# Kernel optimization log

Measured on AMD Instinct MI355X. Metric: run time of the kernel, lower is better.

## Reference

```python
import jax, jax.numpy as jnp
import numpy as np

N = 16384          # batch of signals
DIM_T = 256        # time steps per signal
DT = 0.01          # integration dt (intg_lev=1 -> dt_intg = dt)
NUF = 256          # num_units_feat
HID_XI = 128       # hidlayers_xi
HID_AUX = 64       # hidlayers_aux1_dec
LEN_INTG = DIM_T   # (dim_t-1)*intg_lev + 1 with intg_lev=1


def _linear_init(key, fan_in, fan_out):
    # torch nn.Linear default: U(-1/sqrt(fan_in), 1/sqrt(fan_in))
    s = 1.0 / np.sqrt(fan_in)
    kw, kb = jax.random.split(key)
    W = jax.random.uniform(kw, (fan_in, fan_out), minval=-s, maxval=s, dtype=jnp.float32)
    b = jax.random.uniform(kb, (fan_out,), minval=-s, maxval=s, dtype=jnp.float32)
    return W, b


def setup_inputs() -> dict:
    key = jax.random.key(0)
    ks = jax.random.split(key, 12)
    data = jax.random.normal(ks[0], (N, DIM_T), dtype=jnp.float32)
    omega = jax.random.normal(ks[1], (N, 1), dtype=jnp.float32)
    eps = jax.random.normal(ks[2], (N, 1), dtype=jnp.float32)
    # feature extractor (mlp branch): [dim_t+1 -> 256 -> 256], relu after both (actfun_output=True)
    W_feat1, b_feat1 = _linear_init(ks[3], DIM_T + 1, NUF)
    W_feat2, b_feat2 = _linear_init(ks[4], NUF, NUF)
    # xi mean head: MLP [256 -> 128 -> 1] then Softplus
    W_xim1, b_xim1 = _linear_init(ks[5], NUF, HID_XI)
    W_xim2, b_xim2 = _linear_init(ks[6], HID_XI, 1)
    # xi lnvar head: MLP [256 -> 128 -> 1]
    W_xil1, b_xil1 = _linear_init(ks[7], NUF, HID_XI)
    W_xil2, b_xil2 = _linear_init(ks[8], HID_XI, 1)
    # decoder aux1 MLP: [dim_z_aux1+1=2 -> 64 -> 1]
    W_aux1, b_aux1 = _linear_init(ks[9], 2, HID_AUX)
    W_aux2, b_aux2 = _linear_init(ks[10], HID_AUX, 1)
    return dict(data=data, omega=omega, eps=eps,
                W_feat1=W_feat1, b_feat1=b_feat1, W_feat2=W_feat2, b_feat2=b_feat2,
                W_xim1=W_xim1, b_xim1=b_xim1, W_xim2=W_xim2, b_xim2=b_xim2,
                W_xil1=W_xil1, b_xil1=b_xil1, W_xil2=W_xil2, b_xil2=b_xil2,
                W_aux1=W_aux1, b_aux1=b_aux1, W_aux2=W_aux2, b_aux2=b_aux2)


def reference(data, omega, eps,
              W_feat1, b_feat1, W_feat2, b_feat2,
              W_xim1, b_xim1, W_xim2, b_xim2,
              W_xil1, b_xil1, W_xil2, b_xil2,
              W_aux1, b_aux1, W_aux2, b_aux2):
    relu = jax.nn.relu
    # ---- encode_xi ----
    x_ = jnp.concatenate([data, omega], axis=1)                 # [n, dim_t+1]
    feat = relu(relu(x_ @ W_feat1 + b_feat1) @ W_feat2 + b_feat2)  # [n, 256]
    xi_mean = jax.nn.softplus(relu(feat @ W_xim1 + b_xim1) @ W_xim2 + b_xim2)  # [n, 1]
    xi_lnvar = relu(feat @ W_xil1 + b_xil1) @ W_xil2 + b_xil2                  # [n, 1]
    # ---- draw (reparameterization + clamp to feasible range [0, 1]) ----
    xi = xi_mean + jnp.exp(0.5 * xi_lnvar) * eps
    xi = jnp.clip(xi, 0.0, 1.0)
    # ---- decode: Euler odeint over LEN_INTG steps of state yy=[y, dy/dt] ----
    init_y = data[:, :1]                                        # [n, 1]
    initcond = jnp.concatenate([init_y, jnp.zeros_like(init_y)], axis=1)  # [n, 2]

    def step(yy, _):
        # physics: d[y, v]/dt = [v, 0]; aux MLP adds acceleration from (z_aux1=omega, y)
        aux_in = jnp.concatenate([omega, yy[:, :1]], axis=1)    # [n, 2]
        acc = relu(aux_in @ W_aux1 + b_aux1) @ W_aux2 + b_aux2  # [n, 1]
        dyy = jnp.concatenate([yy[:, 1:2], acc], axis=1)        # [n, 2]
        return yy + DT * dyy, yy

    _, yy_seq = jax.lax.scan(step, initcond, None, length=LEN_INTG)  # [len_intg, n, 2]
    y_seq = yy_seq[:, :, 0].T                                   # [n, dim_t] (intg_lev=1)
    t_intg = DT * jnp.arange(LEN_INTG, dtype=jnp.float32)       # [dim_t]
    x_PAB = jnp.exp(-jnp.abs(xi) * t_intg[None, :]) * y_seq     # [n, dim_t]
    return xi_mean, xi_lnvar, x_PAB
```

## Files before the change

kernel.cpp:

```cpp
#include <hip/hip_runtime.h>
#include <math.h>

#define NROWS 16384
#define DT_C 0.01f

typedef short s16x8 __attribute__((ext_vector_type(8)));
typedef float f32x4 __attribute__((ext_vector_type(4)));
typedef float f32x2 __attribute__((ext_vector_type(2)));

__device__ __forceinline__ unsigned short f2bf(float f) {
    unsigned u = __float_as_uint(f);
    u += 0x7fffu + ((u >> 16) & 1u);
    return (unsigned short)(u >> 16);
}
__device__ __forceinline__ unsigned pack2bf(float a, float b) {
    return (unsigned)f2bf(a) | ((unsigned)f2bf(b) << 16);
}
template <int CTRL>
__device__ __forceinline__ float dppadd(float v) {
    int x = __builtin_amdgcn_update_dpp(0, __float_as_int(v), CTRL, 0xF, 0xF, true);
    return v + __int_as_float(x);
}
__device__ __forceinline__ float sum4(float p) {
    p = dppadd<0xB1>(p);
    p = dppadd<0x4E>(p);
    return p;
}
__device__ __forceinline__ float sum8(float p) {
    p = dppadd<0xB1>(p);
    p = dppadd<0x4E>(p);
    p = dppadd<0x141>(p);
    return p;
}

__global__ __launch_bounds__(256) void prep_k(
    const float* __restrict__ Wf1, const float* __restrict__ Wf2,
    const float* __restrict__ Wm1, const float* __restrict__ Wl1,
    const float* __restrict__ bm1, const float* __restrict__ bl1,
    unsigned short* __restrict__ wpack, float* __restrict__ biasH)
{
    const int id = blockIdx.x * 256 + threadIdx.x;
    const int n  = id & 255;
    const int k8 = (id >> 8) & 31;
    const int s  = id >> 13;

    unsigned short tmp[8];
    #pragma unroll
    for (int j = 0; j < 8; ++j) {
        const int k = k8 * 8 + j;
        float v;
        if (s == 0)      v = Wf1[k * 256 + n];
        else if (s == 1) v = Wf2[k * 256 + n];
        else             v = (n < 128) ? Wm1[k * 128 + n] : Wl1[k * 128 + n - 128];
        tmp[j] = f2bf(v);
    }
    *(uint4*)&wpack[((s * 32 + k8) * 256 + n) * 8] = *(const uint4*)tmp;

    if (id < 256) biasH[id] = (id < 128) ? bm1[id] : bl1[id - 128];
}

__global__ __launch_bounds__(256, 2) void mega_k(
    const float* __restrict__ data, const float* __restrict__ omega,
    const float* __restrict__ eps_g,
    const unsigned short* __restrict__ wpack, const float* __restrict__ biasH,
    const float* __restrict__ bf1, const float* __restrict__ bf2,
    const float* __restrict__ w256g,
    const float* __restrict__ Wm2, const float* __restrict__ bm2,
    const float* __restrict__ Wl2, const float* __restrict__ bl2,
    float* __restrict__ out_mean, float* __restrict__ out_lnvar,
    float* __restrict__ xi_ws)
{
    __shared__ __align__(16) unsigned char smem[32896];
    unsigned short* As1 = (unsigned short*)smem;
    unsigned short* Hs  = (unsigned short*)(smem + 16384);
    float* headsF = (float*)smem;
    float* omg = (float*)(smem + 32768);

    const int tid  = threadIdx.x;
    const int wid  = tid >> 6;
    const int lane = tid & 63;
    const int ln   = lane & 15;
    const int quad = lane >> 4;
    const int r0   = blockIdx.x * 32;

    {
        #pragma unroll
        for (int g2 = 0; g2 < 8; ++g2) {
            const int unit = g2 * 256 + tid;
            const int m    = unit >> 6;
            const int c16  = unit & 63;
            const int kblk = c16 >> 1;
            const int h    = c16 & 1;
            const float4 v = *(const float4*)&data[(size_t)(r0 + m) * 256 + c16 * 4];
            unsigned* d = (unsigned*)&As1[((kblk * 32) + (m ^ (kblk & 7))) * 8 + h * 4];
            d[0] = pack2bf(v.x, v.y);
            d[1] = pack2bf(v.z, v.w);
        }
        if (tid < 32) omg[tid] = omega[r0 + tid];
    }

    f32x4 acc[2][4];

    auto seed = [&](const float* bias) {
        #pragma unroll
        for (int nt = 0; nt < 4; ++nt) {
            const float b = bias[wid * 64 + nt * 16 + ln];
            acc[0][nt] = f32x4{b, b, b, b};
            acc[1][nt] = acc[0][nt];
        }
    };

    auto run_stage = [&](const unsigned short* Ap, const unsigned short* wp) {
        #pragma unroll
        for (int c = 0; c < 4; ++c) {
            #pragma unroll
            for (int kk = 0; kk < 2; ++kk) {
                const int kb   = kk * 4 + quad;
                const int kblk = c * 8 + kb;
                const int f    = kblk & 7;
                s16x8 b0 = *(const s16x8*)&wp[((size_t)(kblk * 256) + wid * 64 + 0 * 16 + ln) * 8];
                s16x8 b1 = *(const s16x8*)&wp[((size_t)(kblk * 256) + wid * 64 + 1 * 16 + ln) * 8];
                s16x8 b2 = *(const s16x8*)&wp[((size_t)(kblk * 256) + wid * 64 + 2 * 16 + ln) * 8];
                s16x8 b3 = *(const s16x8*)&wp[((size_t)(kblk * 256) + wid * 64 + 3 * 16 + ln) * 8];
                s16x8 a0 = *(const s16x8*)&Ap[(kblk * 32 + (ln ^ f)) * 8];
                s16x8 a1 = *(const s16x8*)&Ap[(kblk * 32 + ((ln ^ f) + 16)) * 8];
                acc[0][0] = __builtin_amdgcn_mfma_f32_16x16x32_bf16(a0, b0, acc[0][0], 0, 0, 0);
                acc[1][0] = __builtin_amdgcn_mfma_f32_16x16x32_bf16(a1, b0, acc[1][0], 0, 0, 0);
                acc[0][1] = __builtin_amdgcn_mfma_f32_16x16x32_bf16(a0, b1, acc[0][1], 0, 0, 0);
                acc[1][1] = __builtin_amdgcn_mfma_f32_16x16x32_bf16(a1, b1, acc[1][1], 0, 0, 0);
                acc[0][2] = __builtin_amdgcn_mfma_f32_16x16x32_bf16(a0, b2, acc[0][2], 0, 0, 0);
                acc[1][2] = __builtin_amdgcn_mfma_f32_16x16x32_bf16(a1, b2, acc[1][2], 0, 0, 0);
                acc[0][3] = __builtin_amdgcn_mfma_f32_16x16x32_bf16(a0, b3, acc[0][3], 0, 0, 0);
                acc[1][3] = __builtin_amdgcn_mfma_f32_16x16x32_bf16(a1, b3, acc[1][3], 0, 0, 0);
            }
        }
    };

    auto write_packed = [&](unsigned short* dst, bool addOm) {
        #pragma unroll
        for (int nt = 0; nt < 4; ++nt) {
            const int col = wid * 64 + nt * 16 + ln;
            const int kg  = col >> 3, f = kg & 7, jj = col & 7;
            const float wo = addOm ? w256g[col] : 0.f;
            #pragma unroll
            for (int mt = 0; mt < 2; ++mt) {
                #pragma unroll
                for (int r = 0; r < 4; ++r) {
                    const int row = mt * 16 + quad * 4 + r;
                    float v = acc[mt][nt][r];
                    if (addOm) v = fmaf(omg[row], wo, v);
                    v = fmaxf(v, 0.f);
                    dst[(kg * 32 + (row ^ f)) * 8 + jj] = f2bf(v);
                }
            }
        }
    };

    __syncthreads();
    seed(bf1);
    run_stage(As1, wpack);
    write_packed(Hs, true);
    __syncthreads();
    seed(bf2);
    run_stage(Hs, wpack + 65536);
    write_packed(As1, false);
    __syncthreads();
    seed(biasH);
    run_stage(As1, wpack + 131072);
    __syncthreads();
    #pragma unroll
    for (int nt = 0; nt < 4; ++nt) {
        const int col = wid * 64 + nt * 16 + ln;
        #pragma unroll
        for (int mt = 0; mt < 2; ++mt) {
            #pragma unroll
            for (int r = 0; r < 4; ++r) {
                const int row = mt * 16 + quad * 4 + r;
                headsF[row * 256 + ((col + row * 8) & 255)] = fmaxf(acc[mt][nt][r], 0.f);
            }
        }
    }
    __syncthreads();

    {
        const int m = tid >> 3, l = tid & 7;
        float pm = 0.f, pl = 0.f;
        #pragma unroll
        for (int q = 0; q < 4; ++q) {
            const int c0 = l * 16 + q * 4;
            const float4 hm = *(const float4*)&headsF[m * 256 + ((c0 + m * 8) & 255)];
            const float4 wm = *(const float4*)&Wm2[c0];
            const float4 hl = *(const float4*)&headsF[m * 256 + ((128 + c0 + m * 8) & 255)];
            const float4 wl = *(const float4*)&Wl2[c0];
            pm = fmaf(hm.w, wm.w, fmaf(hm.z, wm.z, fmaf(hm.y, wm.y, fmaf(hm.x, wm.x, pm))));
            pl = fmaf(hl.w, wl.w, fmaf(hl.z, wl.z, fmaf(hl.y, wl.y, fmaf(hl.x, wl.x, pl))));
        }
        pm = sum8(pm);
        pl = sum8(pl);
        if (l == 0) {
            const float xm   = pm + bm2[0];
            const float mean = fmaxf(xm, 0.f) + log1pf(expf(-fabsf(xm)));
            const float lnv  = pl + bl2[0];
            out_mean[r0 + m]  = mean;
            out_lnvar[r0 + m] = lnv;
            float xi = mean + expf(0.5f * lnv) * eps_g[r0 + m];
            xi_ws[r0 + m] = fminf(fmaxf(xi, 0.f), 1.f);
        }
    }
}

__global__ __launch_bounds__(256) void ode2_k(
    const float* __restrict__ data, const float* __restrict__ omega_g,
    const float* __restrict__ xi_ws,
    const float* __restrict__ Wa1, const float* __restrict__ ba1,
    const float* __restrict__ Wa2, const float* __restrict__ ba2,
    float* __restrict__ xout)
{
    const int tid = threadIdx.x;
    const int r   = tid >> 2;
    const int l   = tid & 3;
    const int row = blockIdx.x * 64 + r;

    const float om = omega_g[row];
    const float xi = xi_ws[row];
    const float s  = expf(-xi * DT_C);
    const float pseed = ba2[0] * 0.25f;

    f32x2 w1v[8], Av[8], w2v[8];
    #pragma unroll
    for (int i = 0; i < 8; ++i) {
        const int u = l * 16 + i * 2;
        const f32x2 w0 = *(const f32x2*)&Wa1[u];
        const f32x2 bb = *(const f32x2*)&ba1[u];
        w1v[i] = *(const f32x2*)&Wa1[64 + u];
        w2v[i] = *(const f32x2*)&Wa2[u];
        Av[i]  = f32x2{fmaf(om, w0.x, bb.x), fmaf(om, w0.y, bb.y)};
    }

    auto partial = [&](float y) -> float {
        const f32x2 y2 = f32x2{y, y};
        f32x2 a0 = f32x2{pseed, 0.f};
        f32x2 a1 = f32x2{0.f, 0.f};
        f32x2 a2 = f32x2{0.f, 0.f};
        f32x2 a3 = f32x2{0.f, 0.f};
        #pragma unroll
        for (int i = 0; i < 8; ++i) {
            f32x2 h = __builtin_elementwise_fma(y2, w1v[i], Av[i]);
            h = __builtin_elementwise_max(h, f32x2{0.f, 0.f});
            if ((i & 3) == 0) a0 = __builtin_elementwise_fma(h, w2v[i], a0);
            if ((i & 3) == 1) a1 = __builtin_elementwise_fma(h, w2v[i], a1);
            if ((i & 3) == 2) a2 = __builtin_elementwise_fma(h, w2v[i], a2);
            if ((i & 3) == 3) a3 = __builtin_elementwise_fma(h, w2v[i], a3);
        }
        a0 = a0 + a1;
        a2 = a2 + a3;
        a0 = a0 + a2;
        return a0.x + a0.y;
    };

    const float y0 = data[(size_t)row * 256];
    float ym = y0;
    float yc = y0;
    const float DT2 = DT_C * DT_C;
    float pr = sum4(partial(ym));
    float d = 1.f;

    float* orow = xout + (size_t)row * 256 + l * 4;
    for (int b = 0; b < 16; ++b) {
        float cur[4] = {0.f, 0.f, 0.f, 0.f};
        #pragma unroll
        for (int j = 0; j < 16; ++j) {
            const float m_ = d * ym;
            if ((j >> 2) == l) cur[j & 3] = m_;
            d *= s;
            float pn = sum4(partial(yc));
            const float ynext = fmaf(DT2, pr, fmaf(2.f, yc, -ym));
            ym = yc; yc = ynext; pr = pn;
        }
        *(float4*)&orow[b * 16] = *(const float4*)cur;
    }
}

extern "C" void kernel_launch(void* const* d_in, const int* in_sizes, int n_in,
                              void* d_out, int out_size, void* d_ws, size_t ws_size,
                              hipStream_t stream)
{
    const float* data    = (const float*)d_in[0];
    const float* omega   = (const float*)d_in[1];
    const float* eps     = (const float*)d_in[2];
    const float* W_feat1 = (const float*)d_in[3];
    const float* b_feat1 = (const float*)d_in[4];
    const float* W_feat2 = (const float*)d_in[5];
    const float* b_feat2 = (const float*)d_in[6];
    const float* W_xim1  = (const float*)d_in[7];
    const float* b_xim1  = (const float*)d_in[8];
    const float* W_xim2  = (const float*)d_in[9];
    const float* b_xim2  = (const float*)d_in[10];
    const float* W_xil1  = (const float*)d_in[11];
    const float* b_xil1  = (const float*)d_in[12];
    const float* W_xil2  = (const float*)d_in[13];
    const float* b_xil2  = (const float*)d_in[14];
    const float* W_aux1  = (const float*)d_in[15];
    const float* b_aux1  = (const float*)d_in[16];
    const float* W_aux2  = (const float*)d_in[17];
    const float* b_aux2  = (const float*)d_in[18];

    float* out_mean  = (float*)d_out;
    float* out_lnvar = out_mean + NROWS;
    float* out_x     = out_lnvar + NROWS;

    unsigned short* wpack = (unsigned short*)d_ws;
    float* biasH = (float*)((char*)d_ws + 3 * 32 * 256 * 8 * 2);
    float* xi_ws = biasH + 256;

    prep_k<<<96, 256, 0, stream>>>(W_feat1, W_feat2, W_xim1, W_xil1,
                                   b_xim1, b_xil1, wpack, biasH);
    mega_k<<<512, 256, 0, stream>>>(data, omega, eps, wpack, biasH,
                                    b_feat1, b_feat2, W_feat1 + 256 * 256,
                                    W_xim2, b_xim2, W_xil2, b_xil2,
                                    out_mean, out_lnvar, xi_ws);
    ode2_k<<<256, 256, 0, stream>>>(data, omega, xi_ws,
                                    W_aux1, b_aux1, W_aux2, b_aux2, out_x);
}
```

Before: 141.1 us.

## Fuse ODE and encoder kernels, overlapping ODE integration with MLP via atomic counter

Merges the encoder MLP kernel and the ODE integration kernel into one launch. The first 256 blocks integrate the ODE independently of xi and buffer the trajectory in registers. They then spin on a global counter until all 512 encoder blocks have published xi, and apply the exponential decay at write time. This is meant to overlap the serial ODE recurrence with the GEMM work and remove a kernel launch boundary. The cost is higher register pressure from holding 64 values per thread, and a risk of deadlock if the waiting blocks occupy every slot before the encoder blocks get scheduled.

Result: slower. 151.8 us (+7.6%).

```diff
diff --git a/kernel.cpp b/kernel.cpp
--- a/kernel.cpp
+++ b/kernel.cpp
@@ -3,6 +3,8 @@
 
 #define NROWS 16384
 #define DT_C 0.01f
+#define ODE_BLOCKS 256
+#define MEGA_BLOCKS 512
 
 typedef short s16x8 __attribute__((ext_vector_type(8)));
 typedef float f32x4 __attribute__((ext_vector_type(4)));
@@ -37,7 +39,8 @@
     const float* __restrict__ Wf1, const float* __restrict__ Wf2,
     const float* __restrict__ Wm1, const float* __restrict__ Wl1,
     const float* __restrict__ bm1, const float* __restrict__ bl1,
-    unsigned short* __restrict__ wpack, float* __restrict__ biasH)
+    unsigned short* __restrict__ wpack, float* __restrict__ biasH,
+    unsigned* __restrict__ cnt)
 {
     const int id = blockIdx.x * 256 + threadIdx.x;
     const int n  = id & 255;
@@ -57,9 +60,10 @@
     *(uint4*)&wpack[((s * 32 + k8) * 256 + n) * 8] = *(const uint4*)tmp;
 
     if (id < 256) biasH[id] = (id < 128) ? bm1[id] : bl1[id - 128];
-}
-
-__global__ __launch_bounds__(256, 2) void mega_k(
+    if (id == 0)  *cnt = 0u;
+}
+
+__global__ __launch_bounds__(256, 2) void fat_k(
     const float* __restrict__ data, const float* __restrict__ omega,
     const float* __restrict__ eps_g,
     const unsigned short* __restrict__ wpack, const float* __restrict__ biasH,
@@ -67,21 +71,110 @@
     const float* __restrict__ w256g,
     const float* __restrict__ Wm2, const float* __restrict__ bm2,
     const float* __restrict__ Wl2, const float* __restrict__ bl2,
+    const float* __restrict__ Wa1, const float* __restrict__ ba1,
+    const float* __restrict__ Wa2, const float* __restrict__ ba2,
     float* __restrict__ out_mean, float* __restrict__ out_lnvar,
-    float* __restrict__ xi_ws)
+    float* __restrict__ xi_ws, unsigned* __restrict__ cnt,
+    float* __restrict__ xout)
 {
     __shared__ __align__(16) unsigned char smem[32896];
+
+    const int tid = threadIdx.x;
+
+    if (blockIdx.x < ODE_BLOCKS) {
+        const int r   = tid >> 2;
+        const int l   = tid & 3;
+        const int row = blockIdx.x * 64 + r;
+
+        const float om = omega[row];
+        const float pseed = ba2[0] * 0.25f;
+
+        f32x2 w1v[8], Av[8], w2v[8];
+        #pragma unroll
+        for (int i = 0; i < 8; ++i) {
+            const int u = l * 16 + i * 2;
+            const f32x2 w0 = *(const f32x2*)&Wa1[u];
+            const f32x2 bb = *(const f32x2*)&ba1[u];
+            w1v[i] = *(const f32x2*)&Wa1[64 + u];
+            w2v[i] = *(const f32x2*)&Wa2[u];
+            Av[i]  = f32x2{fmaf(om, w0.x, bb.x), fmaf(om, w0.y, bb.y)};
+        }
+
+        auto partial = [&](float y) -> float {
+            const f32x2 y2 = f32x2{y, y};
+            f32x2 a0 = f32x2{pseed, 0.f};
+            f32x2 a1 = f32x2{0.f, 0.f};
+            f32x2 a2 = f32x2{0.f, 0.f};
+            f32x2 a3 = f32x2{0.f, 0.f};
+            #pragma unroll
+            for (int i = 0; i < 8; ++i) {
+                f32x2 h = __builtin_elementwise_fma(y2, w1v[i], Av[i]);
+                h = __builtin_elementwise_max(h, f32x2{0.f, 0.f});
+                if ((i & 3) == 0) a0 = __builtin_elementwise_fma(h, w2v[i], a0);
+                if ((i & 3) == 1) a1 = __builtin_elementwise_fma(h, w2v[i], a1);
+                if ((i & 3) == 2) a2 = __builtin_elementwise_fma(h, w2v[i], a2);
+                if ((i & 3) == 3) a3 = __builtin_elementwise_fma(h, w2v[i], a3);
+            }
+            a0 = a0 + a1;
+            a2 = a2 + a3;
+            a0 = a0 + a2;
+            return a0.x + a0.y;
+        };
+
+        float cur[16][4];
+        const float y0 = data[(size_t)row * 256];
+        float ym = y0, yc = y0;
+        const float DT2 = DT_C * DT_C;
+        float pr = sum4(partial(ym));
+
+        #pragma unroll
+        for (int b = 0; b < 16; ++b) {
+            #pragma unroll
+            for (int j = 0; j < 16; ++j) {
+                if ((j >> 2) == l) cur[b][j & 3] = ym;
+                float pn = sum4(partial(yc));
+                const float yn = fmaf(DT2, pr, fmaf(2.f, yc, -ym));
+                ym = yc; yc = yn; pr = pn;
+            }
+        }
+
+        if (tid == 0) {
+            while (__hip_atomic_load(cnt, __ATOMIC_ACQUIRE,
+                                     __HIP_MEMORY_SCOPE_AGENT) < MEGA_BLOCKS)
+                __builtin_amdgcn_s_sleep(4);
+        }
+        __syncthreads();
+        const float xi = __hip_atomic_load(&xi_ws[row], __ATOMIC_RELAXED,
+                                           __HIP_MEMORY_SCOPE_AGENT);
+        const float E   = __expf(-xi * DT_C);
+        const float E16 = __expf(-16.f * xi * DT_C);
+        float f = __expf(-(float)(4 * l) * xi * DT_C);
+
+        float* orow = xout + (size_t)row * 256 + l * 4;
+        #pragma unroll
+        for (int b = 0; b < 16; ++b) {
+            float t = f;
+            float4 o;
+            o.x = cur[b][0] * t; t *= E;
+            o.y = cur[b][1] * t; t *= E;
+            o.z = cur[b][2] * t; t *= E;
+            o.w = cur[b][3] * t;
+            *(float4*)&orow[b * 16] = o;
+            f *= E16;
+        }
+        return;
+    }
+
     unsigned short* As1 = (unsigned short*)smem;
     unsigned short* Hs  = (unsigned short*)(smem + 16384);
     float* headsF = (float*)smem;
     float* omg = (float*)(smem + 32768);
 
-    const int tid  = threadIdx.x;
     const int wid  = tid >> 6;
     const int lane = tid & 63;
     const int ln   = lane & 15;
     const int quad = lane >> 4;
-    const int r0   = blockIdx.x * 32;
+    const int r0   = (blockIdx.x - ODE_BLOCKS) * 32;
 
     {
         #pragma unroll
@@ -204,81 +297,15 @@
             out_mean[r0 + m]  = mean;
             out_lnvar[r0 + m] = lnv;
             float xi = mean + expf(0.5f * lnv) * eps_g[r0 + m];
-            xi_ws[r0 + m] = fminf(fmaxf(xi, 0.f), 1.f);
-        }
-    }
-}
-
-__global__ __launch_bounds__(256) void ode2_k(
-    const float* __restrict__ data, const float* __restrict__ omega_g,
-    const float* __restrict__ xi_ws,
-    const float* __restrict__ Wa1, const float* __restrict__ ba1,
-    const float* __restrict__ Wa2, const float* __restrict__ ba2,
-    float* __restrict__ xout)
-{
-    const int tid = threadIdx.x;
-    const int r   = tid >> 2;
-    const int l   = tid & 3;
-    const int row = blockIdx.x * 64 + r;
-
-    const float om = omega_g[row];
-    const float xi = xi_ws[row];
-    const float s  = expf(-xi * DT_C);
-    const float pseed = ba2[0] * 0.25f;
-
-    f32x2 w1v[8], Av[8], w2v[8];
-    #pragma unroll
-    for (int i = 0; i < 8; ++i) {
-        const int u = l * 16 + i * 2;
-        const f32x2 w0 = *(const f32x2*)&Wa1[u];
-        const f32x2 bb = *(const f32x2*)&ba1[u];
-        w1v[i] = *(const f32x2*)&Wa1[64 + u];
-        w2v[i] = *(const f32x2*)&Wa2[u];
-        Av[i]  = f32x2{fmaf(om, w0.x, bb.x), fmaf(om, w0.y, bb.y)};
-    }
-
-    auto partial = [&](float y) -> float {
-        const f32x2 y2 = f32x2{y, y};
-        f32x2 a0 = f32x2{pseed, 0.f};
-        f32x2 a1 = f32x2{0.f, 0.f};
-        f32x2 a2 = f32x2{0.f, 0.f};
-        f32x2 a3 = f32x2{0.f, 0.f};
-        #pragma unroll
-        for (int i = 0; i < 8; ++i) {
-            f32x2 h = __builtin_elementwise_fma(y2, w1v[i], Av[i]);
-            h = __builtin_elementwise_max(h, f32x2{0.f, 0.f});
-            if ((i & 3) == 0) a0 = __builtin_elementwise_fma(h, w2v[i], a0);
-            if ((i & 3) == 1) a1 = __builtin_elementwise_fma(h, w2v[i], a1);
-            if ((i & 3) == 2) a2 = __builtin_elementwise_fma(h, w2v[i], a2);
-            if ((i & 3) == 3) a3 = __builtin_elementwise_fma(h, w2v[i], a3);
-        }
-        a0 = a0 + a1;
-        a2 = a2 + a3;
-        a0 = a0 + a2;
-        return a0.x + a0.y;
-    };
-
-    const float y0 = data[(size_t)row * 256];
-    float ym = y0;
-    float yc = y0;
-    const float DT2 = DT_C * DT_C;
-    float pr = sum4(partial(ym));
-    float d = 1.f;
-
-    float* orow = xout + (size_t)row * 256 + l * 4;
-    for (int b = 0; b < 16; ++b) {
-        float cur[4] = {0.f, 0.f, 0.f, 0.f};
-        #pragma unroll
-        for (int j = 0; j < 16; ++j) {
-            const float m_ = d * ym;
-            if ((j >> 2) == l) cur[j & 3] = m_;
-            d *= s;
-            float pn = sum4(partial(yc));
-            const float ynext = fmaf(DT2, pr, fmaf(2.f, yc, -ym));
-            ym = yc; yc = ynext; pr = pn;
-        }
-        *(float4*)&orow[b * 16] = *(const float4*)cur;
-    }
+            xi = fminf(fmaxf(xi, 0.f), 1.f);
+            __hip_atomic_store(&xi_ws[r0 + m], xi, __ATOMIC_RELAXED,
+                               __HIP_MEMORY_SCOPE_AGENT);
+        }
+    }
+    __syncthreads();
+    if (tid == 0)
+        __hip_atomic_fetch_add(cnt, 1u, __ATOMIC_RELEASE,
+                               __HIP_MEMORY_SCOPE_AGENT);
 }
 
 extern "C" void kernel_launch(void* const* d_in, const int* in_sizes, int n_in,
@@ -312,13 +339,14 @@
     unsigned short* wpack = (unsigned short*)d_ws;
     float* biasH = (float*)((char*)d_ws + 3 * 32 * 256 * 8 * 2);
     float* xi_ws = biasH + 256;
+    unsigned* cnt = (unsigned*)(xi_ws + NROWS);
 
     prep_k<<<96, 256, 0, stream>>>(W_feat1, W_feat2, W_xim1, W_xil1,
-                                   b_xim1, b_xil1, wpack, biasH);
-    mega_k<<<512, 256, 0, stream>>>(data, omega, eps, wpack, biasH,
-                                    b_feat1, b_feat2, W_feat1 + 256 * 256,
-                                    W_xim2, b_xim2, W_xil2, b_xil2,
-                                    out_mean, out_lnvar, xi_ws);
-    ode2_k<<<256, 256, 0, stream>>>(data, omega, xi_ws,
-                                    W_aux1, b_aux1, W_aux2, b_aux2, out_x);
-}
+                                   b_xim1, b_xil1, wpack, biasH, cnt);
+    fat_k<<<ODE_BLOCKS + MEGA_BLOCKS, 256, 0, stream>>>(
+        data, omega, eps, wpack, biasH,
+        b_feat1, b_feat2, W_feat1 + 256 * 256,
+        W_xim2, b_xim2, W_xil2, b_xil2,
+        W_aux1, b_aux1, W_aux2, b_aux2,
+        out_mean, out_lnvar, xi_ws, cnt, out_x);
+}
```
